# Kernel tuning notes

Hardware: AMD Instinct MI355X
Metric: run time of the kernel (lower is better)

## Reference

```python
import jax, jax.numpy as jnp
import numpy as np

N_NODES = 50000
N_EDGES = 800000
IN_FEATS = 64
H_FEATS = 128


def _uniform(key, shape, stdv):
    return jax.random.uniform(key, shape, jnp.float32, -stdv, stdv)


def setup_inputs() -> dict:
    key = jax.random.key(0)
    ks = jax.random.split(key, 16)
    inp = {}
    inp["features"] = jax.random.normal(ks[0], (N_NODES, IN_FEATS), jnp.float32)
    inp["mask"] = (jax.random.uniform(ks[1], (N_NODES, IN_FEATS)) > 0.3).astype(jnp.float32)
    inp["norm_g"] = jax.random.uniform(ks[2], (N_NODES, 1), jnp.float32, 0.05, 1.0)
    inp["norm_f"] = jax.random.uniform(ks[3], (N_NODES, 1), jnp.float32, 0.05, 1.0)
    inp["src_g"] = jax.random.randint(ks[4], (N_EDGES,), 0, N_NODES, jnp.int32)
    inp["dst_g"] = jax.random.randint(ks[5], (N_EDGES,), 0, N_NODES, jnp.int32)
    inp["src_f"] = jax.random.randint(ks[6], (N_EDGES,), 0, N_NODES, jnp.int32)
    inp["dst_f"] = jax.random.randint(ks[7], (N_EDGES,), 0, N_NODES, jnp.int32)
    # learned params, init per reset_parameters (uniform +/- 1/sqrt(out_feats))
    s1 = 1.0 / np.sqrt(H_FEATS)
    inp["W1"] = _uniform(ks[8], (IN_FEATS, H_FEATS), s1)
    inp["b1"] = _uniform(ks[9], (H_FEATS,), s1)
    s2 = 1.0 / np.sqrt(IN_FEATS)
    inp["wh"] = _uniform(ks[10], (H_FEATS, IN_FEATS), s2)
    inp["bh"] = _uniform(ks[11], (IN_FEATS,), s2)
    inp["ws"] = _uniform(ks[12], (IN_FEATS, IN_FEATS), s2)
    inp["bs"] = _uniform(ks[13], (IN_FEATS,), s2)
    return inp


def _aggregate(h, src, dst):
    # DGL update_all(copy_src, sum): gather source node feats per edge, sum at dst
    return jax.ops.segment_sum(h[src], dst, num_segments=N_NODES)


def reference(features, mask, norm_g, norm_f, src_g, dst_g, src_f, dst_f,
              W1, b1, wh, bh, ws, bs):
    x = features * mask                     # [N, in]
    # GCL (masked_gcn)
    h = (x @ W1) * norm_g                   # [N, h]
    h = _aggregate(h, src_g, dst_g) * norm_g + b1
    h = jax.nn.relu(h)
    # GCL_skip (output_gcn): h branch on g, skip branch s on f
    hb = (h @ wh) * norm_g                  # [N, in]
    sb = (x @ ws) * norm_f                  # [N, in]
    hb = _aggregate(hb, src_g, dst_g) * norm_g + bh
    sb = _aggregate(sb, src_f, dst_f) * norm_f + bs
    return jax.nn.sigmoid(hb + sb)
```

## Files before the change

### kernel.cpp

```cpp
#include <hip/hip_runtime.h>
#include <hip/hip_fp16.h>

#define N_NODES 50000
#define N_EDGES 800000
#define IN_F 64
#define H_F 128
#define NBUK 49
#define EPB 2048
#define NBLK 391
#define CAP 24576

typedef unsigned short u16;
typedef unsigned int u32;

static __device__ __forceinline__ float4 ld4(const float* p) {
    return *reinterpret_cast<const float4*>(p);
}
static __device__ __forceinline__ void st4(float* p, float4 v) {
    *reinterpret_cast<float4*>(p) = v;
}
static __device__ __forceinline__ void st_h4(__half* p, float4 v) {
    union { __half h[4]; uint2 u; } pk;
    pk.h[0] = __float2half_rn(v.x);
    pk.h[1] = __float2half_rn(v.y);
    pk.h[2] = __float2half_rn(v.z);
    pk.h[3] = __float2half_rn(v.w);
    *reinterpret_cast<uint2*>(p) = pk.u;
}
static __device__ __forceinline__ void add_h8(float4& a, float4& b, uint4 r) {
    __half2* p = reinterpret_cast<__half2*>(&r);
    float2 f0 = __half22float2(p[0]);
    float2 f1 = __half22float2(p[1]);
    float2 f2 = __half22float2(p[2]);
    float2 f3 = __half22float2(p[3]);
    a.x += f0.x; a.y += f0.y; a.z += f1.x; a.w += f1.y;
    b.x += f2.x; b.y += f2.y; b.z += f3.x; b.w += f3.y;
}

__global__ __launch_bounds__(256) void part_k(
    const int* __restrict__ src_g, const int* __restrict__ dst_g, u32* __restrict__ rec_g,
    const int* __restrict__ src_f, const int* __restrict__ dst_f, u32* __restrict__ rec_f,
    int* __restrict__ bukcur,
    const float* __restrict__ f, const float* __restrict__ m,
    const float* __restrict__ ng, __half* __restrict__ y)
{
    __shared__ int c[NBUK];
    __shared__ int base[NBUK];
    const int tid = threadIdx.x;
    const int graph = blockIdx.x >= NBLK;
    const int blk = blockIdx.x - graph * NBLK;
    const int* src = graph ? src_f : src_g;
    const int* dst = graph ? dst_f : dst_g;
    u32* rec = graph ? rec_f : rec_g;
    int* cur = bukcur + graph * NBUK;

    if (tid < NBUK) c[tid] = 0;
    __syncthreads();
    const int e0 = blk * EPB;
    const int e1 = min(e0 + EPB, N_EDGES);

    u32 r_[8];
    bool v_[8];
#pragma unroll
    for (int j = 0; j < 8; ++j) {
        int e = e0 + tid + j * 256;
        v_[j] = (e < e1);
        int d = 0, s = 0;
        if (v_[j]) { d = dst[e]; s = src[e]; }
        r_[j] = ((u32)s << 16) | (u32)d;
        if (v_[j]) atomicAdd(&c[d >> 10], 1);
    }
    __syncthreads();
    if (tid < NBUK) base[tid] = atomicAdd(&cur[tid], c[tid]);
    __syncthreads();
    if (tid < NBUK) c[tid] = 0;
    __syncthreads();
#pragma unroll
    for (int j = 0; j < 8; ++j) {
        if (v_[j]) {
            u32 r = r_[j];
            int b = (int)((r & 0xFFFFu) >> 10);
            int p = base[b] + atomicAdd(&c[b], 1);
            if (p < CAP) rec[b * CAP + p] = r;
        }
    }
    for (int i = blockIdx.x * 256 + tid; i < N_NODES * (IN_F / 4);
         i += gridDim.x * 256) {
        int n = i >> 4;
        float s = ng[n];
        float4 a = ld4(f + 4 * i);
        float4 b = ld4(m + 4 * i);
        float4 r;
        r.x = a.x * b.x * s; r.y = a.y * b.y * s;
        r.z = a.z * b.z * s; r.w = a.w * b.w * s;
        st_h4(y + 4 * i, r);
    }
}

__global__ __launch_bounds__(1024) void p3_build_k(
    const u32* __restrict__ rec_g, int* __restrict__ rps_g, int* __restrict__ rpe_g,
    u16* __restrict__ adj_g,
    const u32* __restrict__ rec_f, int* __restrict__ rps_f, int* __restrict__ rpe_f,
    u16* __restrict__ adj_f,
    const int* __restrict__ bukcur)
{
    __shared__ int hist[1024];
    __shared__ int tmp[1024];
    const int tid = threadIdx.x;
    const int graph = blockIdx.x >= NBUK;
    const int b = blockIdx.x - graph * NBUK;
    const u32* rec = graph ? rec_f : rec_g;
    int* rps = graph ? rps_f : rps_g;
    int* rpe = graph ? rpe_f : rpe_g;
    u16* adj = graph ? adj_f : adj_g;
    const int e_base = b * CAP;
    const int e_cnt  = min(bukcur[graph * NBUK + b], CAP);

    hist[tid] = 0;
    __syncthreads();
    for (int i = tid; i < e_cnt; i += 1024)
        atomicAdd(&hist[rec[e_base + i] & 1023], 1);
    __syncthreads();
    const int v = hist[tid];
    tmp[tid] = v;
    __syncthreads();
    for (int o = 1; o < 1024; o <<= 1) {
        int t = (tid >= o) ? tmp[tid - o] : 0;
        __syncthreads();
        tmp[tid] += t;
        __syncthreads();
    }
    const int incl = tmp[tid];
    const int excl = incl - v;
    const int n = (b << 10) + tid;
    if (n < N_NODES) {
        rps[n] = e_base + excl;
        rpe[n] = e_base + incl;
    }
    hist[tid] = excl;
    __syncthreads();
    for (int i = tid; i < e_cnt; i += 1024) {
        u32 r = rec[e_base + i];
        int p = atomicAdd(&hist[r & 1023], 1);
        adj[e_base + p] = (u16)(r >> 16);
    }
}

static __device__ __forceinline__ void csr_row_sum_h8(
        const __half* __restrict__ tbl, const u16* __restrict__ adj,
        int e, int e1, int off, float4& A, float4& B) {
    for (; e + 4 <= e1; e += 4) {
        int s0 = adj[e], s1 = adj[e + 1], s2 = adj[e + 2], s3 = adj[e + 3];
        uint4 r0 = *reinterpret_cast<const uint4*>(tbl + (s0 << 6) + off);
        uint4 r1 = *reinterpret_cast<const uint4*>(tbl + (s1 << 6) + off);
        uint4 r2 = *reinterpret_cast<const uint4*>(tbl + (s2 << 6) + off);
        uint4 r3 = *reinterpret_cast<const uint4*>(tbl + (s3 << 6) + off);
        add_h8(A, B, r0); add_h8(A, B, r1); add_h8(A, B, r2); add_h8(A, B, r3);
    }
    for (; e < e1; ++e) {
        uint4 r = *reinterpret_cast<const uint4*>(tbl + (adj[e] << 6) + off);
        add_h8(A, B, r);
    }
}

__global__ __launch_bounds__(256) void agg64_k(const __half* __restrict__ tbl,
        const int* __restrict__ rps, const int* __restrict__ rpe,
        const u16* __restrict__ adj, float* __restrict__ out) {
    const int tid = threadIdx.x;
    const int fl = tid & 7;
    const int n  = blockIdx.x * 32 + (tid >> 3);
    if (n >= N_NODES) return;
    const int off = fl << 3;
    float4 A = make_float4(0.f, 0.f, 0.f, 0.f);
    float4 B = make_float4(0.f, 0.f, 0.f, 0.f);
    csr_row_sum_h8(tbl, adj, rps[n], rpe[n], off, A, B);
    st4(out + (n << 6) + off, A);
    st4(out + (n << 6) + off + 4, B);
}

template<int K, int N, int SMODE, int EPI, int OUT16>
__global__ __launch_bounds__(256) void gemm_k(
    const float* __restrict__ A, const float* __restrict__ A2,
    const float* __restrict__ W, const float* __restrict__ rs,
    const float* __restrict__ bias, void* __restrict__ outv, int M)
{
    constexpr int CPT = N / 16;
    constexpr int AS  = K + 1;
    constexpr int KQ  = K / 4;
    __shared__ __align__(16) float Wl[K * N];
    __shared__ __align__(16) float Al[64 * AS];

    const int tid = threadIdx.x;
    const int n0  = blockIdx.x << 6;

    for (int i = tid; i < K * N / 4; i += 256) st4(&Wl[4 * i], ld4(W + 4 * i));
    for (int i4 = tid; i4 < 64 * KQ; i4 += 256) {
        int n  = i4 / KQ;
        int k4 = (i4 & (KQ - 1)) << 2;
        int gn = n0 + n;
        float4 v = make_float4(0.f, 0.f, 0.f, 0.f);
        if (gn < M) {
            v = ld4(A + gn * K + k4);
            if (SMODE == 1) {
                float4 m4 = ld4(A2 + gn * K + k4);
                v.x *= m4.x; v.y *= m4.y; v.z *= m4.z; v.w *= m4.w;
            }
        }
        float* p = &Al[n * AS + k4];
        p[0] = v.x; p[1] = v.y; p[2] = v.z; p[3] = v.w;
    }
    __syncthreads();

    const int tr = tid & 15;
    const int tc = tid >> 4;

    float acc[4][CPT];
#pragma unroll
    for (int i = 0; i < 4; ++i)
#pragma unroll
        for (int j = 0; j < CPT; ++j) acc[i][j] = 0.f;

#pragma unroll 4
    for (int k = 0; k < K; ++k) {
        float a0 = Al[(4 * tr + 0) * AS + k];
        float a1 = Al[(4 * tr + 1) * AS + k];
        float a2 = Al[(4 * tr + 2) * AS + k];
        float a3 = Al[(4 * tr + 3) * AS + k];
#pragma unroll
        for (int jq = 0; jq < CPT / 4; ++jq) {
            float4 w = ld4(&Wl[k * N + tc * CPT + 4 * jq]);
            acc[0][4 * jq + 0] += a0 * w.x; acc[0][4 * jq + 1] += a0 * w.y;
            acc[0][4 * jq + 2] += a0 * w.z; acc[0][4 * jq + 3] += a0 * w.w;
            acc[1][4 * jq + 0] += a1 * w.x; acc[1][4 * jq + 1] += a1 * w.y;
            acc[1][4 * jq + 2] += a1 * w.z; acc[1][4 * jq + 3] += a1 * w.w;
            acc[2][4 * jq + 0] += a2 * w.x; acc[2][4 * jq + 1] += a2 * w.y;
            acc[2][4 * jq + 2] += a2 * w.z; acc[2][4 * jq + 3] += a2 * w.w;
            acc[3][4 * jq + 0] += a3 * w.x; acc[3][4 * jq + 1] += a3 * w.y;
            acc[3][4 * jq + 2] += a3 * w.z; acc[3][4 * jq + 3] += a3 * w.w;
        }
    }

#pragma unroll
    for (int i = 0; i < 4; ++i) {
        int gn = n0 + 4 * tr + i;
        if (gn >= M) continue;
        float s = rs[gn];
#pragma unroll
        for (int jq = 0; jq < CPT / 4; ++jq) {
            float4 o;
            if (EPI == 1) {
                float4 b4 = ld4(bias + tc * CPT + 4 * jq);
                o.x = fmaxf(fmaf(acc[i][4 * jq + 0], s, b4.x), 0.f);
                o.y = fmaxf(fmaf(acc[i][4 * jq + 1], s, b4.y), 0.f);
                o.z = fmaxf(fmaf(acc[i][4 * jq + 2], s, b4.z), 0.f);
                o.w = fmaxf(fmaf(acc[i][4 * jq + 3], s, b4.w), 0.f);
            } else {
                o.x = acc[i][4 * jq + 0] * s; o.y = acc[i][4 * jq + 1] * s;
                o.z = acc[i][4 * jq + 2] * s; o.w = acc[i][4 * jq + 3] * s;
            }
            if (OUT16) {
                st_h4((__half*)outv + gn * N + tc * CPT + 4 * jq, o);
            } else {
                st4((float*)outv + gn * N + tc * CPT + 4 * jq, o);
            }
        }
    }
}

__global__ __launch_bounds__(256) void final2_k(
    const __half* __restrict__ hb, const __half* __restrict__ sb,
    const int* __restrict__ rps_g, const int* __restrict__ rpe_g,
    const u16* __restrict__ adj_g,
    const int* __restrict__ rps_f, const int* __restrict__ rpe_f,
    const u16* __restrict__ adj_f,
    const float* __restrict__ ng, const float* __restrict__ nf,
    const float* __restrict__ bh, const float* __restrict__ bs,
    float* __restrict__ out)
{
    const int tid = threadIdx.x;
    const int fl = tid & 7;
    const int n  = blockIdx.x * 32 + (tid >> 3);
    if (n >= N_NODES) return;
    const int off = fl << 3;
    float4 Ag = make_float4(0.f, 0.f, 0.f, 0.f);
    float4 Bg = make_float4(0.f, 0.f, 0.f, 0.f);
    float4 Af = make_float4(0.f, 0.f, 0.f, 0.f);
    float4 Bf = make_float4(0.f, 0.f, 0.f, 0.f);
    csr_row_sum_h8(hb, adj_g, rps_g[n], rpe_g[n], off, Ag, Bg);
    csr_row_sum_h8(sb, adj_f, rps_f[n], rpe_f[n], off, Af, Bf);
    const float g = ng[n], f = nf[n];
    float4 b0 = ld4(bh + off), b1 = ld4(bh + off + 4);
    float4 s0 = ld4(bs + off), s1 = ld4(bs + off + 4);
    float4 o0, o1;
    float t;
    t = Ag.x * g + b0.x + Af.x * f + s0.x; o0.x = 1.f / (1.f + expf(-t));
    t = Ag.y * g + b0.y + Af.y * f + s0.y; o0.y = 1.f / (1.f + expf(-t));
    t = Ag.z * g + b0.z + Af.z * f + s0.z; o0.z = 1.f / (1.f + expf(-t));
    t = Ag.w * g + b0.w + Af.w * f + s0.w; o0.w = 1.f / (1.f + expf(-t));
    t = Bg.x * g + b1.x + Bf.x * f + s1.x; o1.x = 1.f / (1.f + expf(-t));
    t = Bg.y * g + b1.y + Bf.y * f + s1.y; o1.y = 1.f / (1.f + expf(-t));
    t = Bg.z * g + b1.z + Bf.z * f + s1.z; o1.z = 1.f / (1.f + expf(-t));
    t = Bg.w * g + b1.w + Bf.w * f + s1.w; o1.w = 1.f / (1.f + expf(-t));
    st4(out + (n << 6) + off, o0);
    st4(out + (n << 6) + off + 4, o1);
}

extern "C" void kernel_launch(void* const* d_in, const int* in_sizes, int n_in,
                              void* d_out, int out_size, void* d_ws, size_t ws_size,
                              hipStream_t stream) {
    const float* features = (const float*)d_in[0];
    const float* mask     = (const float*)d_in[1];
    const float* norm_g   = (const float*)d_in[2];
    const float* norm_f   = (const float*)d_in[3];
    const int*   src_g    = (const int*)d_in[4];
    const int*   dst_g    = (const int*)d_in[5];
    const int*   src_f    = (const int*)d_in[6];
    const int*   dst_f    = (const int*)d_in[7];
    const float* W1  = (const float*)d_in[8];
    const float* b1  = (const float*)d_in[9];
    const float* wh  = (const float*)d_in[10];
    const float* bh  = (const float*)d_in[11];
    const float* wsw = (const float*)d_in[12];
    const float* bs  = (const float*)d_in[13];
    float* out = (float*)d_out;
    float* ws  = (float*)d_ws;

    __half* y   = (__half*)ws;
    float*  z   = ws + 3200000;
    float*  t1  = ws + 6400000;
    __half* hb0 = (__half*)ws;
    __half* sb0 = (__half*)(ws + 3200000);
    int* creg   = (int*)(ws + 6400000);
    u32* rec_g  = (u32*)creg;
    u32* rec_f  = (u32*)(creg + NBUK * CAP);
    int* bukcur = creg + 2 * NBUK * CAP;
    int* pers   = (int*)(ws + 12800000);
    int* rps_g  = pers;
    int* rpe_g  = pers + 50000;
    int* rps_f  = pers + 100000;
    int* rpe_f  = pers + 150000;
    u16* adj_g  = (u16*)(pers + 200000);
    u16* adj_f  = adj_g + NBUK * CAP;

    const int gblocks = (N_NODES + 63) / 64;
    const int nblk32  = (N_NODES + 31) / 32;

    hipMemsetAsync(bukcur, 0, 2 * NBUK * sizeof(int), stream);
    part_k<<<2 * NBLK, 256, 0, stream>>>(src_g, dst_g, rec_g,
                                         src_f, dst_f, rec_f, bukcur,
                                         features, mask, norm_g, y);
    p3_build_k<<<2 * NBUK, 1024, 0, stream>>>(rec_g, rps_g, rpe_g, adj_g,
                                              rec_f, rps_f, rpe_f, adj_f, bukcur);

    agg64_k<<<nblk32, 256, 0, stream>>>(y, rps_g, rpe_g, adj_g, z);

    gemm_k<64, 128, 0, 1, 0><<<gblocks, 256, 0, stream>>>(z, nullptr, W1, norm_g,
                                                          b1, (void*)t1, N_NODES);
    gemm_k<128, 64, 0, 2, 1><<<gblocks, 256, 0, stream>>>(t1, nullptr, wh, norm_g,
                                                          nullptr, (void*)hb0, N_NODES);
    gemm_k<64, 64, 1, 2, 1><<<gblocks, 256, 0, stream>>>(features, mask, wsw, norm_f,
                                                         nullptr, (void*)sb0, N_NODES);

    final2_k<<<nblk32, 256, 0, stream>>>(hb0, sb0, rps_g, rpe_g, adj_g,
                                         rps_f, rpe_f, adj_f,
                                         norm_g, norm_f, bh, bs, out);
}
```

Measured before the change: 247.5 us.

## Fuse first aggregation with both dense layers; halve bucket width in CSR build

Replaces the separate aggregation kernel and the two GEMM kernels for the h branch with one kernel. Each block gathers neighbor rows for 64 nodes into shared memory, runs the 64x128 layer with bias and ReLU, keeps the hidden tile in half precision in shared memory, then runs the 128x64 layer and writes hb0. This removes the fp32 z and t1 round trips through global memory and two launches. Separately, the CSR bucketing moves to 512-node buckets (98 buckets, 512-thread build blocks) to give the build kernel more parallelism. The cost is lower occupancy from the large shared-memory footprint, a gather phase that uses only 4 threads per node, and rounding of the hidden activations to fp16.

After: 250.0 us. Within noise of the previous version (+1.0%).

```diff
diff --git a/kernel.cpp b/kernel.cpp
--- a/kernel.cpp
+++ b/kernel.cpp
@@ -5,10 +5,10 @@
 #define N_EDGES 800000
 #define IN_F 64
 #define H_F 128
-#define NBUK 49
+#define NBUK 98
+#define CAPB 12288
 #define EPB 2048
 #define NBLK 391
-#define CAP 24576
 
 typedef unsigned short u16;
 typedef unsigned int u32;
@@ -68,7 +68,7 @@
         int d = 0, s = 0;
         if (v_[j]) { d = dst[e]; s = src[e]; }
         r_[j] = ((u32)s << 16) | (u32)d;
-        if (v_[j]) atomicAdd(&c[d >> 10], 1);
+        if (v_[j]) atomicAdd(&c[d >> 9], 1);
     }
     __syncthreads();
     if (tid < NBUK) base[tid] = atomicAdd(&cur[tid], c[tid]);
@@ -79,9 +79,9 @@
     for (int j = 0; j < 8; ++j) {
         if (v_[j]) {
             u32 r = r_[j];
-            int b = (int)((r & 0xFFFFu) >> 10);
+            int b = (int)((r & 0xFFFFu) >> 9);
             int p = base[b] + atomicAdd(&c[b], 1);
-            if (p < CAP) rec[b * CAP + p] = r;
+            if (p < CAPB) rec[b * CAPB + p] = r;
         }
     }
     for (int i = blockIdx.x * 256 + tid; i < N_NODES * (IN_F / 4);
@@ -97,15 +97,15 @@
     }
 }
 
-__global__ __launch_bounds__(1024) void p3_build_k(
+__global__ __launch_bounds__(512) void p3_build_k(
     const u32* __restrict__ rec_g, int* __restrict__ rps_g, int* __restrict__ rpe_g,
     u16* __restrict__ adj_g,
     const u32* __restrict__ rec_f, int* __restrict__ rps_f, int* __restrict__ rpe_f,
     u16* __restrict__ adj_f,
     const int* __restrict__ bukcur)
 {
-    __shared__ int hist[1024];
-    __shared__ int tmp[1024];
+    __shared__ int hist[512];
+    __shared__ int tmp[512];
     const int tid = threadIdx.x;
     const int graph = blockIdx.x >= NBUK;
     const int b = blockIdx.x - graph * NBUK;
@@ -113,18 +113,18 @@
     int* rps = graph ? rps_f : rps_g;
     int* rpe = graph ? rpe_f : rpe_g;
     u16* adj = graph ? adj_f : adj_g;
-    const int e_base = b * CAP;
-    const int e_cnt  = min(bukcur[graph * NBUK + b], CAP);
+    const int e_base = b * CAPB;
+    const int e_cnt  = min(bukcur[graph * NBUK + b], CAPB);
 
     hist[tid] = 0;
     __syncthreads();
-    for (int i = tid; i < e_cnt; i += 1024)
-        atomicAdd(&hist[rec[e_base + i] & 1023], 1);
+    for (int i = tid; i < e_cnt; i += 512)
+        atomicAdd(&hist[rec[e_base + i] & 511], 1);
     __syncthreads();
     const int v = hist[tid];
     tmp[tid] = v;
     __syncthreads();
-    for (int o = 1; o < 1024; o <<= 1) {
+    for (int o = 1; o < 512; o <<= 1) {
         int t = (tid >= o) ? tmp[tid - o] : 0;
         __syncthreads();
         tmp[tid] += t;
@@ -132,17 +132,156 @@
     }
     const int incl = tmp[tid];
     const int excl = incl - v;
-    const int n = (b << 10) + tid;
+    const int n = (b << 9) + tid;
     if (n < N_NODES) {
         rps[n] = e_base + excl;
         rpe[n] = e_base + incl;
     }
     hist[tid] = excl;
     __syncthreads();
-    for (int i = tid; i < e_cnt; i += 1024) {
+    for (int i = tid; i < e_cnt; i += 512) {
         u32 r = rec[e_base + i];
-        int p = atomicAdd(&hist[r & 1023], 1);
+        int p = atomicAdd(&hist[r & 511], 1);
         adj[e_base + p] = (u16)(r >> 16);
+    }
+}
+
+__global__ __launch_bounds__(256) void fused_mlp_k(
+    const __half* __restrict__ y,
+    const int* __restrict__ rps, const int* __restrict__ rpe,
+    const u16* __restrict__ adj,
+    const float* __restrict__ W1, const float* __restrict__ b1,
+    const float* __restrict__ wh, const float* __restrict__ ng,
+    __half* __restrict__ hb0, int M)
+{
+    __shared__ __align__(16) float  Wl[8192];
+    __shared__ __align__(16) float  Al[64 * 68];
+    __shared__ __align__(16) __half Ah[64 * 136];
+
+    const int tid = threadIdx.x;
+    const int n0  = blockIdx.x << 6;
+
+    for (int i = tid; i < 2048; i += 256) st4(&Wl[4 * i], ld4(W1 + 4 * i));
+
+    {
+        const int node = tid >> 2, q = tid & 3;
+        const int gn = n0 + node;
+        float4 A0 = make_float4(0.f, 0.f, 0.f, 0.f);
+        float4 A1 = make_float4(0.f, 0.f, 0.f, 0.f);
+        float4 A2 = make_float4(0.f, 0.f, 0.f, 0.f);
+        float4 A3 = make_float4(0.f, 0.f, 0.f, 0.f);
+        if (gn < M) {
+            int e = rps[gn];
+            const int e1 = rpe[gn];
+            const __half* base = y + (q << 4);
+            for (; e + 2 <= e1; e += 2) {
+                const __half* ra = base + ((int)adj[e] << 6);
+                const __half* rb = base + ((int)adj[e + 1] << 6);
+                uint4 a0 = *reinterpret_cast<const uint4*>(ra);
+                uint4 a1 = *reinterpret_cast<const uint4*>(ra + 8);
+                uint4 b0 = *reinterpret_cast<const uint4*>(rb);
+                uint4 b1v = *reinterpret_cast<const uint4*>(rb + 8);
+                add_h8(A0, A1, a0); add_h8(A2, A3, a1);
+                add_h8(A0, A1, b0); add_h8(A2, A3, b1v);
+            }
+            for (; e < e1; ++e) {
+                const __half* ra = base + ((int)adj[e] << 6);
+                uint4 a0 = *reinterpret_cast<const uint4*>(ra);
+                uint4 a1 = *reinterpret_cast<const uint4*>(ra + 8);
+                add_h8(A0, A1, a0); add_h8(A2, A3, a1);
+            }
+        }
+        float* p = &Al[node * 68 + (q << 4)];
+        st4(p, A0); st4(p + 4, A1); st4(p + 8, A2); st4(p + 12, A3);
+    }
+    __syncthreads();
+
+    const int tr = tid & 15;
+    const int tc = tid >> 4;
+    float ngv[4];
+#pragma unroll
+    for (int i = 0; i < 4; ++i) {
+        int gn = n0 + 4 * tr + i;
+        ngv[i] = (gn < M) ? ng[gn] : 0.f;
+    }
+
+    float acc1[4][8];
+#pragma unroll
+    for (int i = 0; i < 4; ++i)
+#pragma unroll
+        for (int j = 0; j < 8; ++j) acc1[i][j] = 0.f;
+#pragma unroll 4
+    for (int k = 0; k < 64; ++k) {
+        float a0 = Al[(4 * tr + 0) * 68 + k];
+        float a1 = Al[(4 * tr + 1) * 68 + k];
+        float a2 = Al[(4 * tr + 2) * 68 + k];
+        float a3 = Al[(4 * tr + 3) * 68 + k];
+#pragma unroll
+        for (int jq = 0; jq < 2; ++jq) {
+            float4 w = ld4(&Wl[k * 128 + tc * 8 + 4 * jq]);
+            acc1[0][4 * jq + 0] += a0 * w.x; acc1[0][4 * jq + 1] += a0 * w.y;
+            acc1[0][4 * jq + 2] += a0 * w.z; acc1[0][4 * jq + 3] += a0 * w.w;
+            acc1[1][4 * jq + 0] += a1 * w.x; acc1[1][4 * jq + 1] += a1 * w.y;
+            acc1[1][4 * jq + 2] += a1 * w.z; acc1[1][4 * jq + 3] += a1 * w.w;
+            acc1[2][4 * jq + 0] += a2 * w.x; acc1[2][4 * jq + 1] += a2 * w.y;
+            acc1[2][4 * jq + 2] += a2 * w.z; acc1[2][4 * jq + 3] += a2 * w.w;
+            acc1[3][4 * jq + 0] += a3 * w.x; acc1[3][4 * jq + 1] += a3 * w.y;
+            acc1[3][4 * jq + 2] += a3 * w.z; acc1[3][4 * jq + 3] += a3 * w.w;
+        }
+    }
+    __syncthreads();
+
+    {
+        float4 bA = ld4(b1 + tc * 8);
+        float4 bB = ld4(b1 + tc * 8 + 4);
+#pragma unroll
+        for (int i = 0; i < 4; ++i) {
+            union { __half h[8]; uint4 u; } pk;
+            float s = ngv[i];
+            pk.h[0] = __float2half_rn(fmaxf(fmaf(acc1[i][0], s, bA.x), 0.f));
+            pk.h[1] = __float2half_rn(fmaxf(fmaf(acc1[i][1], s, bA.y), 0.f));
+            pk.h[2] = __float2half_rn(fmaxf(fmaf(acc1[i][2], s, bA.z), 0.f));
+            pk.h[3] = __float2half_rn(fmaxf(fmaf(acc1[i][3], s, bA.w), 0.f));
+            pk.h[4] = __float2half_rn(fmaxf(fmaf(acc1[i][4], s, bB.x), 0.f));
+            pk.h[5] = __float2half_rn(fmaxf(fmaf(acc1[i][5], s, bB.y), 0.f));
+            pk.h[6] = __float2half_rn(fmaxf(fmaf(acc1[i][6], s, bB.z), 0.f));
+            pk.h[7] = __float2half_rn(fmaxf(fmaf(acc1[i][7], s, bB.w), 0.f));
+            *reinterpret_cast<uint4*>(&Ah[(4 * tr + i) * 136 + tc * 8]) = pk.u;
+        }
+        for (int i = tid; i < 2048; i += 256) st4(&Wl[4 * i], ld4(wh + 4 * i));
+    }
+    __syncthreads();
+
+    float acc2[4][4];
+#pragma unroll
+    for (int i = 0; i < 4; ++i)
+#pragma unroll
+        for (int j = 0; j < 4; ++j) acc2[i][j] = 0.f;
+#pragma unroll 4
+    for (int k = 0; k < 128; ++k) {
+        float a0 = __half2float(Ah[(4 * tr + 0) * 136 + k]);
+        float a1 = __half2float(Ah[(4 * tr + 1) * 136 + k]);
+        float a2 = __half2float(Ah[(4 * tr + 2) * 136 + k]);
+        float a3 = __half2float(Ah[(4 * tr + 3) * 136 + k]);
+        float4 w = ld4(&Wl[k * 64 + tc * 4]);
+        acc2[0][0] += a0 * w.x; acc2[0][1] += a0 * w.y;
+        acc2[0][2] += a0 * w.z; acc2[0][3] += a0 * w.w;
+        acc2[1][0] += a1 * w.x; acc2[1][1] += a1 * w.y;
+        acc2[1][2] += a1 * w.z; acc2[1][3] += a1 * w.w;
+        acc2[2][0] += a2 * w.x; acc2[2][1] += a2 * w.y;
+        acc2[2][2] += a2 * w.z; acc2[2][3] += a2 * w.w;
+        acc2[3][0] += a3 * w.x; acc2[3][1] += a3 * w.y;
+        acc2[3][2] += a3 * w.z; acc2[3][3] += a3 * w.w;
+    }
+#pragma unroll
+    for (int i = 0; i < 4; ++i) {
+        int gn = n0 + 4 * tr + i;
+        if (gn >= M) continue;
+        float s = ngv[i];
+        float4 o;
+        o.x = acc2[i][0] * s; o.y = acc2[i][1] * s;
+        o.z = acc2[i][2] * s; o.w = acc2[i][3] * s;
+        st_h4(hb0 + (gn << 6) + tc * 4, o);
     }
 }
 
@@ -161,21 +300,6 @@
         uint4 r = *reinterpret_cast<const uint4*>(tbl + (adj[e] << 6) + off);
         add_h8(A, B, r);
     }
-}
-
-__global__ __launch_bounds__(256) void agg64_k(const __half* __restrict__ tbl,
-        const int* __restrict__ rps, const int* __restrict__ rpe,
-        const u16* __restrict__ adj, float* __restrict__ out) {
-    const int tid = threadIdx.x;
-    const int fl = tid & 7;
-    const int n  = blockIdx.x * 32 + (tid >> 3);
-    if (n >= N_NODES) return;
-    const int off = fl << 3;
-    float4 A = make_float4(0.f, 0.f, 0.f, 0.f);
-    float4 B = make_float4(0.f, 0.f, 0.f, 0.f);
-    csr_row_sum_h8(tbl, adj, rps[n], rpe[n], off, A, B);
-    st4(out + (n << 6) + off, A);
-    st4(out + (n << 6) + off + 4, B);
 }
 
 template<int K, int N, int SMODE, int EPI, int OUT16>
@@ -326,21 +450,19 @@
     float* ws  = (float*)d_ws;
 
     __half* y   = (__half*)ws;
-    float*  z   = ws + 3200000;
-    float*  t1  = ws + 6400000;
-    __half* hb0 = (__half*)ws;
+    __half* hb0 = (__half*)(ws + 1600000);
     __half* sb0 = (__half*)(ws + 3200000);
     int* creg   = (int*)(ws + 6400000);
     u32* rec_g  = (u32*)creg;
-    u32* rec_f  = (u32*)(creg + NBUK * CAP);
-    int* bukcur = creg + 2 * NBUK * CAP;
+    u32* rec_f  = rec_g + NBUK * CAPB;
+    int* bukcur = (int*)(rec_f + NBUK * CAPB);
     int* pers   = (int*)(ws + 12800000);
     int* rps_g  = pers;
     int* rpe_g  = pers + 50000;
     int* rps_f  = pers + 100000;
     int* rpe_f  = pers + 150000;
     u16* adj_g  = (u16*)(pers + 200000);
-    u16* adj_f  = adj_g + NBUK * CAP;
+    u16* adj_f  = adj_g + NBUK * CAPB;
 
     const int gblocks = (N_NODES + 63) / 64;
     const int nblk32  = (N_NODES + 31) / 32;
@@ -349,15 +471,12 @@
     part_k<<<2 * NBLK, 256, 0, stream>>>(src_g, dst_g, rec_g,
                                          src_f, dst_f, rec_f, bukcur,
                                          features, mask, norm_g, y);
-    p3_build_k<<<2 * NBUK, 1024, 0, stream>>>(rec_g, rps_g, rpe_g, adj_g,
-                                              rec_f, rps_f, rpe_f, adj_f, bukcur);
-
-    agg64_k<<<nblk32, 256, 0, stream>>>(y, rps_g, rpe_g, adj_g, z);
-
-    gemm_k<64, 128, 0, 1, 0><<<gblocks, 256, 0, stream>>>(z, nullptr, W1, norm_g,
-                                                          b1, (void*)t1, N_NODES);
-    gemm_k<128, 64, 0, 2, 1><<<gblocks, 256, 0, stream>>>(t1, nullptr, wh, norm_g,
-                                                          nullptr, (void*)hb0, N_NODES);
+    p3_build_k<<<2 * NBUK, 512, 0, stream>>>(rec_g, rps_g, rpe_g, adj_g,
+                                             rec_f, rps_f, rpe_f, adj_f, bukcur);
+
+    fused_mlp_k<<<gblocks, 256, 0, stream>>>(y, rps_g, rpe_g, adj_g,
+                                             W1, b1, wh, norm_g, hb0, N_NODES);
+
     gemm_k<64, 64, 1, 2, 1><<<gblocks, 256, 0, stream>>>(features, mask, wsw, norm_f,
                                                          nullptr, (void*)sb0, N_NODES);
 
```
